# Kernel tuning notes

Measured on AMD Instinct MI355X. Metric: run time of the kernel, lower is better.

Reference implementation:

```python
import jax, jax.numpy as jnp
import numpy as np

B, T, L, W = 4, 4096, 64, 8          # batch, text len, media tokens, max_window_per_audio
DIM, DIM_A, H, DH = 2048, 1024, 8, 64
INNER = H * DH
LN_EPS = 1e-5


def setup_inputs() -> dict:
    key = jax.random.key(0)
    ks = jax.random.split(key, 8)
    x = jax.random.normal(ks[0], (B, T, DIM), jnp.float32)
    media = jax.random.normal(ks[1], (B, L, 1, DIM_A), jnp.float32)
    media_mask = jax.random.uniform(ks[2], (B, L, 1)) > 0.1
    # sparse media markers (~8 per row); ensure at least one per row
    media_locations = (jax.random.uniform(ks[3], (B, T)) < (8.0 / T)).astype(jnp.int32)
    media_locations = media_locations.at[:, 0].set(1)
    Wq = jax.random.normal(ks[4], (DIM, INNER), jnp.float32) / np.sqrt(DIM).astype(np.float32)
    Wkv = jax.random.normal(ks[5], (DIM_A, 2 * INNER), jnp.float32) / np.sqrt(DIM_A).astype(np.float32)
    Wout = jax.random.normal(ks[6], (INNER, DIM), jnp.float32) / np.sqrt(INNER).astype(np.float32)
    gamma = jnp.ones((DIM,), jnp.float32)
    beta = jnp.zeros((DIM,), jnp.float32)
    return dict(x=x, media=media, media_mask=media_mask, media_locations=media_locations,
                Wq=Wq, Wkv=Wkv, Wout=Wout, gamma=gamma, beta=beta)


def reference(x, media, media_mask, media_locations, Wq, Wkv, Wout, gamma, beta):
    scale = DH ** -0.5
    # LayerNorm (biased variance, like torch)
    mu = x.mean(-1, keepdims=True)
    var = x.var(-1, keepdims=True)
    xn = (x - mu) * jax.lax.rsqrt(var + LN_EPS) * gamma + beta
    # projections
    q = (xn @ Wq).reshape(B, T, H, DH).transpose(0, 2, 1, 3) * scale   # [B,h,T,dh]
    kv = media.reshape(B, L, DIM_A) @ Wkv
    k, v = jnp.split(kv, 2, axis=-1)
    k = k.reshape(B, L, H, DH).transpose(0, 2, 1, 3)                   # [B,h,L,dh]
    v = v.reshape(B, L, H, DH).transpose(0, 2, 1, 3)
    sim = jnp.einsum('bhid,bhjd->bhij', q, k)                          # [B,h,T,L]
    big = jnp.finfo(sim.dtype).max
    # media validity mask
    mm = media_mask.reshape(B, 1, 1, L)
    sim = jnp.where(mm, sim, -big)
    # few-shot window mask (only_attend_immediate_media=False):
    # token t attends windows [0, max(#media at <=t, 1) * W)
    cum = jnp.cumsum((media_locations != 0).astype(jnp.int32), axis=1)  # [B,T]
    end = jnp.maximum(cum, 1) * W                                       # [B,T]
    fsm = jnp.arange(L)[None, None, :] < end[:, :, None]                # [B,T,L]
    sim = jnp.where(fsm[:, None], sim, -big)
    sim = sim - jax.lax.stop_gradient(sim.max(-1, keepdims=True))
    attn = jax.nn.softmax(sim, axis=-1)
    out = jnp.einsum('bhij,bhjd->bhid', attn, v)                        # [B,h,T,dh]
    out = out.transpose(0, 2, 1, 3).reshape(B, T, INNER)
    return out @ Wout
```

## Files before the change

kernel.cpp:

```cpp
#include <hip/hip_runtime.h>
#include <float.h>

typedef __bf16 bf16;
typedef __bf16 bf16x8 __attribute__((ext_vector_type(8)));
typedef float f32x4 __attribute__((ext_vector_type(4)));

#define GAS __attribute__((address_space(1)))
#define LAS __attribute__((address_space(3)))

__device__ __forceinline__ void gload_lds16(const void* g, void* l) {
  __builtin_amdgcn_global_load_lds((const GAS unsigned int*)g, (LAS unsigned int*)l, 16, 0, 0);
}

__global__ __launch_bounds__(512, 4) void qattn(
    const bf16* __restrict__ xn, const bf16* __restrict__ wqT,
    const bf16* __restrict__ kvb, const int* __restrict__ mk,
    const int* __restrict__ endw, bf16* __restrict__ aob) {
  constexpr int K = 2048;
  __shared__ __align__(16) bf16 Abuf[2][128 * 64];
  __shared__ __align__(16) bf16 Bbuf[2][128 * 64];
  const int tid = threadIdx.x, lane = tid & 63;
  const int w = tid >> 6, wr = w >> 1, wc = w & 1;
  const int g = lane >> 4, fr = lane & 15;

  const int gx = gridDim.x;
  int lid = blockIdx.y * gx + blockIdx.x;
  lid = ((lid & 7) << 6) | (lid >> 3);
  const int bx = lid % gx, by = lid / gx;
  const size_t m0 = (size_t)by * 128;
  const int n0 = bx * 128;
  const int b = by >> 5;

  const int nt = K >> 6;
  const int srow = tid >> 3, sslot = tid & 7;

  f32x4 acc[2][4] = {};

  auto stage = [&](int t) {
    const int s = t & 1;
    const int kt = t << 6;
#pragma unroll
    for (int c = 0; c < 2; ++c) {
      const int r = c * 64 + srow;
      gload_lds16(xn + (m0 + r) * (size_t)K + kt + ((sslot ^ (r & 7)) << 3),
                  &Abuf[s][c * 4096 + tid * 8]);
    }
#pragma unroll
    for (int c = 0; c < 2; ++c) {
      const int r = c * 64 + srow;
      gload_lds16(wqT + (size_t)(n0 + r) * K + kt + ((sslot ^ (r & 7)) << 3),
                  &Bbuf[s][c * 4096 + tid * 8]);
    }
  };
  auto rdA = [&](int s, int mi, int ks) {
    const int r = wr * 32 + mi * 16 + fr;
    return *(const bf16x8*)&Abuf[s][r * 64 + ((((ks << 2) | g) ^ (r & 7)) << 3)];
  };
  auto rdB = [&](int s, int ni, int ks) {
    const int r = wc * 64 + ni * 16 + fr;
    return *(const bf16x8*)&Bbuf[s][r * 64 + ((((ks << 2) | g) ^ (r & 7)) << 3)];
  };
  auto compute = [&](int t) {
    const int s = t & 1;
    bf16x8 bv[4][2];
#pragma unroll
    for (int ni = 0; ni < 4; ++ni)
#pragma unroll
      for (int ks = 0; ks < 2; ++ks) bv[ni][ks] = rdB(s, ni, ks);
    __builtin_amdgcn_s_setprio(1);
#pragma unroll
    for (int mi = 0; mi < 2; ++mi)
#pragma unroll
      for (int ks = 0; ks < 2; ++ks) {
        const bf16x8 av = rdA(s, mi, ks);
#pragma unroll
        for (int ni = 0; ni < 4; ++ni)
          acc[mi][ni] = __builtin_amdgcn_mfma_f32_16x16x32_bf16(
              av, bv[ni][ks], acc[mi][ni], 0, 0, 0);
      }
    __builtin_amdgcn_s_setprio(0);
  };

  stage(0);
  for (int t = 0; t < nt; ++t) {
    __syncthreads();
    if (t + 1 < nt) stage(t + 1);
    compute(t);
  }

  __syncthreads();

  bf16* QP = &Abuf[0][0] + w * 2048;
  bf16* Klds = &Bbuf[0][0];
  bf16* Vlds = &Bbuf[1][0];

#pragma unroll
  for (int mi = 0; mi < 2; ++mi)
#pragma unroll
    for (int ni = 0; ni < 4; ++ni)
#pragma unroll
      for (int rg = 0; rg < 4; ++rg) {
        const int row = mi * 16 + g * 4 + rg, col = ni * 16 + fr;
        QP[row * 64 + (((col >> 3) ^ (row & 7)) << 3) + (col & 7)] =
            (bf16)acc[mi][ni][rg];
      }

#pragma unroll
  for (int j = 0; j < 2; ++j) {
    const int idx = j * 512 + tid;
    const int head = idx >> 9, l = (idx >> 3) & 63, sl = idx & 7;
    gload_lds16(kvb + (size_t)(b * 64 + l) * 1024 + (2 * bx + head) * 64 +
                    ((sl ^ (l & 7)) << 3),
                Klds + (j * 512 + w * 64) * 8);
  }
#pragma unroll
  for (int j = 0; j < 2; ++j) {
    const int idx = j * 512 + tid;
    const int head = idx >> 9, l = (idx >> 3) & 63, sg = idx & 7;
    bf16x8 vv = *(const bf16x8*)&kvb[(size_t)(b * 64 + l) * 1024 + 512 +
                                     (2 * bx + head) * 64 + sg * 8];
#pragma unroll
    for (int e = 0; e < 8; ++e) {
      const int dh = sg * 8 + e;
      Vlds[head * 4096 + dh * 64 + (((l >> 3) ^ (dh & 7)) << 3) + (l & 7)] =
          vv[e];
    }
  }
  asm volatile("s_waitcnt vmcnt(0)" ::: "memory");
  __syncthreads();

  f32x4 sacc[2][4] = {};
#pragma unroll
  for (int ks = 0; ks < 2; ++ks) {
    bf16x8 aq[2], bk[4];
#pragma unroll
    for (int mi = 0; mi < 2; ++mi) {
      const int r = mi * 16 + fr;
      aq[mi] = *(const bf16x8*)&QP[r * 64 + ((((ks << 2) | g) ^ (r & 7)) << 3)];
    }
#pragma unroll
    for (int ni = 0; ni < 4; ++ni) {
      const int l = ni * 16 + fr;
      bk[ni] = *(const bf16x8*)&Klds[wc * 4096 + l * 64 +
                                     ((((ks << 2) | g) ^ (l & 7)) << 3)];
    }
#pragma unroll
    for (int mi = 0; mi < 2; ++mi)
#pragma unroll
      for (int ni = 0; ni < 4; ++ni)
        sacc[mi][ni] = __builtin_amdgcn_mfma_f32_16x16x32_bf16(
            aq[mi], bk[ni], sacc[mi][ni], 0, 0, 0);
  }

#pragma unroll
  for (int mi = 0; mi < 2; ++mi) {
    const int4 ev4 = *(const int4*)&endw[m0 + wr * 32 + mi * 16 + g * 4];
    const int ev[4] = {ev4.x, ev4.y, ev4.z, ev4.w};
    float p[4][4];
#pragma unroll
    for (int ni = 0; ni < 4; ++ni) {
      const int l = ni * 16 + fr;
      const bool mv = (mk[b * 64 + l] != 0);
#pragma unroll
      for (int rg = 0; rg < 4; ++rg)
        p[ni][rg] = (mv && (l < ev[rg])) ? sacc[mi][ni][rg] : -FLT_MAX;
    }
#pragma unroll
    for (int rg = 0; rg < 4; ++rg) {
      float m = fmaxf(fmaxf(p[0][rg], p[1][rg]), fmaxf(p[2][rg], p[3][rg]));
      m = fmaxf(m, __shfl_xor(m, 1));
      m = fmaxf(m, __shfl_xor(m, 2));
      m = fmaxf(m, __shfl_xor(m, 4));
      m = fmaxf(m, __shfl_xor(m, 8));
      float sum = 0.f;
#pragma unroll
      for (int ni = 0; ni < 4; ++ni) {
        p[ni][rg] = __expf(p[ni][rg] - m);
        sum += p[ni][rg];
      }
      sum += __shfl_xor(sum, 1);
      sum += __shfl_xor(sum, 2);
      sum += __shfl_xor(sum, 4);
      sum += __shfl_xor(sum, 8);
      const float inv = 1.f / sum;
#pragma unroll
      for (int ni = 0; ni < 4; ++ni) p[ni][rg] *= inv;
    }
#pragma unroll
    for (int ni = 0; ni < 4; ++ni) {
      const int l = ni * 16 + fr;
#pragma unroll
      for (int rg = 0; rg < 4; ++rg) {
        const int row = mi * 16 + g * 4 + rg;
        QP[row * 64 + (((l >> 3) ^ (row & 7)) << 3) + (l & 7)] =
            (bf16)p[ni][rg];
      }
    }
  }

  f32x4 oacc[2][4] = {};
#pragma unroll
  for (int ks = 0; ks < 2; ++ks) {
    bf16x8 pa[2], bv[4];
#pragma unroll
    for (int mi = 0; mi < 2; ++mi) {
      const int r = mi * 16 + fr;
      pa[mi] = *(const bf16x8*)&QP[r * 64 + ((((ks << 2) | g) ^ (r & 7)) << 3)];
    }
#pragma unroll
    for (int nd = 0; nd < 4; ++nd) {
      const int dh = nd * 16 + fr;
      bv[nd] = *(const bf16x8*)&Vlds[wc * 4096 + dh * 64 +
                                     ((((ks << 2) | g) ^ (dh & 7)) << 3)];
    }
#pragma unroll
    for (int mi = 0; mi < 2; ++mi)
#pragma unroll
      for (int nd = 0; nd < 4; ++nd)
        oacc[mi][nd] = __builtin_amdgcn_mfma_f32_16x16x32_bf16(
            pa[mi], bv[nd], oacc[mi][nd], 0, 0, 0);
  }
#pragma unroll
  for (int mi = 0; mi < 2; ++mi)
#pragma unroll
    for (int nd = 0; nd < 4; ++nd)
#pragma unroll
      for (int rg = 0; rg < 4; ++rg) {
        const size_t t = m0 + wr * 32 + mi * 16 + g * 4 + rg;
        aob[t * 512 + (2 * bx + wc) * 64 + nd * 16 + fr] =
            (bf16)oacc[mi][nd][rg];
      }
}

template <int OUT_BF16>
__global__ __launch_bounds__(256, 2) void gemm_bt(
    const bf16* __restrict__ A, const bf16* __restrict__ Bt,
    void* __restrict__ Cv, int M, int N, int K) {
  __shared__ bf16 As[128 * 32];
  __shared__ bf16 Bs[128 * 32];
  const int tid = threadIdx.x;
  const int lane = tid & 63, w = tid >> 6;
  const int wr = w >> 1, wc = w & 1;

  const int gx = gridDim.x;
  const int nwg = gx * gridDim.y;
  int lid = blockIdx.y * gx + blockIdx.x;
  {
    const int qq = nwg >> 3, rr = nwg & 7;
    const int xcd = lid & 7, pos = lid >> 3;
    lid = (xcd < rr ? xcd * (qq + 1) : rr * (qq + 1) + (xcd - rr) * qq) + pos;
  }
  const int bx = lid % gx, by = lid / gx;
  const size_t m0 = (size_t)by * 128, n0 = (size_t)bx * 128;

  const int srow = lane >> 2, sslot = lane & 3;
  const int g = lane >> 4, fr = lane & 15;

  f32x4 acc[4][4] = {};

  for (int kt = 0; kt < K; kt += 32) {
    __syncthreads();
#pragma unroll
    for (int j = 0; j < 2; ++j) {
      const int c = 2 * w + j;
      const int r = c * 16 + srow;
      const int ks = (sslot ^ (r & 3)) << 3;
      gload_lds16(A + (m0 + r) * K + kt + ks, &As[c * 512]);
      gload_lds16(Bt + (n0 + r) * K + kt + ks, &Bs[c * 512]);
    }
    __syncthreads();
    bf16x8 av[4], bv[4];
#pragma unroll
    for (int mi = 0; mi < 4; ++mi) {
      const int r = wr * 64 + mi * 16 + fr;
      av[mi] = *(const bf16x8*)&As[r * 32 + ((g ^ (r & 3)) << 3)];
    }
#pragma unroll
    for (int ni = 0; ni < 4; ++ni) {
      const int r = wc * 64 + ni * 16 + fr;
      bv[ni] = *(const bf16x8*)&Bs[r * 32 + ((g ^ (r & 3)) << 3)];
    }
#pragma unroll
    for (int mi = 0; mi < 4; ++mi)
#pragma unroll
      for (int ni = 0; ni < 4; ++ni)
        acc[mi][ni] = __builtin_amdgcn_mfma_f32_16x16x32_bf16(
            av[mi], bv[ni], acc[mi][ni], 0, 0, 0);
  }

#pragma unroll
  for (int mi = 0; mi < 4; ++mi)
#pragma unroll
    for (int ni = 0; ni < 4; ++ni)
#pragma unroll
      for (int rg = 0; rg < 4; ++rg) {
        const size_t row = m0 + wr * 64 + mi * 16 + g * 4 + rg;
        const size_t col = n0 + wc * 64 + ni * 16 + fr;
        if (OUT_BF16)
          ((bf16*)Cv)[row * (size_t)N + col] = (bf16)acc[mi][ni][rg];
        else
          ((float*)Cv)[row * (size_t)N + col] = acc[mi][ni][rg];
      }
}

__device__ __forceinline__ void transp64(const float* __restrict__ src,
                                         bf16* __restrict__ dst, int R, int C,
                                         float scale, int tile, float* lds) {
  const int tilesC = C >> 6;
  const int tr = tile / tilesC, tc = tile % tilesC;
  const int r0 = tr << 6, c0 = tc << 6;
  const int tid = threadIdx.x;
  const int lr = tid >> 6, lc = tid & 63;
#pragma unroll
  for (int j = 0; j < 16; ++j) {
    const int r = j * 4 + lr;
    lds[r * 65 + lc] = src[(size_t)(r0 + r) * C + c0 + lc];
  }
  __syncthreads();
#pragma unroll
  for (int j = 0; j < 16; ++j) {
    const int rr = j * 4 + lr;
    dst[(size_t)(c0 + rr) * R + r0 + lc] = (bf16)(lds[lc * 65 + rr] * scale);
  }
}

__global__ __launch_bounds__(256) void prep_all(
    const float* __restrict__ x, const float* __restrict__ gamma,
    const float* __restrict__ beta, bf16* __restrict__ xn,
    const float* __restrict__ Wq, bf16* __restrict__ wqT,
    const float* __restrict__ Wkv, bf16* __restrict__ wkvT,
    const float* __restrict__ Wout, bf16* __restrict__ woT,
    const float* __restrict__ media, bf16* __restrict__ medb,
    const int* __restrict__ mloc, int* __restrict__ endw,
    const unsigned char* __restrict__ mraw, int* __restrict__ mk) {
  __shared__ float shf[64 * 65];
  const int blk = blockIdx.x, tid = threadIdx.x;

  if (blk < 16384) {
    const size_t base = (size_t)blk * 2048 + tid * 8;
    f32x4 v0 = *(const f32x4*)(x + base);
    f32x4 v1 = *(const f32x4*)(x + base + 4);
    float s = 0.f, q2 = 0.f;
#pragma unroll
    for (int j = 0; j < 4; ++j) {
      s += v0[j] + v1[j];
      q2 += v0[j] * v0[j] + v1[j] * v1[j];
    }
    for (int off = 32; off > 0; off >>= 1) {
      s += __shfl_down(s, off);
      q2 += __shfl_down(q2, off);
    }
    const int lane = tid & 63, wv = tid >> 6;
    if (lane == 0) { shf[wv] = s; shf[4 + wv] = q2; }
    __syncthreads();
    s = shf[0] + shf[1] + shf[2] + shf[3];
    q2 = shf[4] + shf[5] + shf[6] + shf[7];
    const float mu = s * (1.f / 2048.f);
    const float var = q2 * (1.f / 2048.f) - mu * mu;
    const float rs = rsqrtf(var + 1e-5f);
    f32x4 g0 = *(const f32x4*)(gamma + tid * 8);
    f32x4 g1 = *(const f32x4*)(gamma + tid * 8 + 4);
    f32x4 b0 = *(const f32x4*)(beta + tid * 8);
    f32x4 b1 = *(const f32x4*)(beta + tid * 8 + 4);
    bf16x8 o;
#pragma unroll
    for (int j = 0; j < 4; ++j) {
      o[j] = (bf16)((v0[j] - mu) * rs * g0[j] + b0[j]);
      o[4 + j] = (bf16)((v1[j] - mu) * rs * g1[j] + b1[j]);
    }
    *(bf16x8*)(xn + base) = o;
  } else if (blk < 16640) {
    transp64(Wq, wqT, 2048, 512, 0.125f, blk - 16384, shf);
  } else if (blk < 16896) {
    transp64(Wkv, wkvT, 1024, 1024, 1.f, blk - 16640, shf);
  } else if (blk < 17152) {
    transp64(Wout, woT, 512, 2048, 1.f, blk - 16896, shf);
  } else if (blk < 18176) {
    const int i = (blk - 17152) * 256 + tid;
    medb[i] = (bf16)media[i];
  } else if (blk < 18180) {
    int* part = (int*)shf;
    const int b = blk - 18176;
    int loc[16];
    int s = 0;
    const int base = b * 4096 + tid * 16;
#pragma unroll
    for (int j = 0; j < 16; ++j) {
      loc[j] = (mloc[base + j] != 0) ? 1 : 0;
      s += loc[j];
    }
    part[tid] = s;
    __syncthreads();
    for (int off = 1; off < 256; off <<= 1) {
      int v = (tid >= off) ? part[tid - off] : 0;
      __syncthreads();
      part[tid] += v;
      __syncthreads();
    }
    int c = (tid > 0) ? part[tid - 1] : 0;
#pragma unroll
    for (int j = 0; j < 16; ++j) {
      c += loc[j];
      int e = (c > 1 ? c : 1) << 3;
      endw[base + j] = e > 64 ? 64 : e;
    }
  } else {
    int* isbool = (int*)shf;
    if (tid == 0) *isbool = 0;
    __syncthreads();
    const unsigned char v = mraw[tid];
    if ((tid & 3) != 0 && v != 0) atomicOr(isbool, 1);
    __syncthreads();
    mk[tid] = (*isbool) ? (int)mraw[tid] : ((const int*)mraw)[tid];
  }
}

extern "C" void kernel_launch(void* const* d_in, const int* in_sizes, int n_in,
                              void* d_out, int out_size, void* d_ws,
                              size_t ws_size, hipStream_t stream) {
  const float* x = (const float*)d_in[0];
  const float* media = (const float*)d_in[1];
  const unsigned char* mraw = (const unsigned char*)d_in[2];
  const int* mloc = (const int*)d_in[3];
  const float* Wq = (const float*)d_in[4];
  const float* Wkv = (const float*)d_in[5];
  const float* Wout = (const float*)d_in[6];
  const float* gamma = (const float*)d_in[7];
  const float* beta = (const float*)d_in[8];
  float* out = (float*)d_out;

  bf16* xn = (bf16*)d_out;

  char* ws = (char*)d_ws;
  size_t off = 0;
  auto carve = [&](size_t bytes) {
    void* p = ws + off;
    off += (bytes + 255) & ~(size_t)255;
    return p;
  };
  bf16* aob = (bf16*)carve((size_t)16384 * 512 * 2);
  bf16* kvb = (bf16*)carve((size_t)256 * 1024 * 2);
  bf16* wqT = (bf16*)carve((size_t)512 * 2048 * 2);
  bf16* wkvT = (bf16*)carve((size_t)1024 * 1024 * 2);
  bf16* woT = (bf16*)carve((size_t)2048 * 512 * 2);
  bf16* medb = (bf16*)carve((size_t)256 * 1024 * 2);
  int* endw = (int*)carve((size_t)4 * 4096 * 4);
  int* mk = (int*)carve(256 * 4);
  (void)ws_size;
  (void)in_sizes;
  (void)n_in;
  (void)out_size;

  prep_all<<<18181, 256, 0, stream>>>(x, gamma, beta, xn, Wq, wqT, Wkv, wkvT,
                                      Wout, woT, media, medb, mloc, endw, mraw,
                                      mk);

  gemm_bt<1><<<dim3(8, 2), 256, 0, stream>>>(medb, wkvT, kvb, 256, 1024, 1024);

  qattn<<<dim3(4, 128), 512, 0, stream>>>(xn, wqT, kvb, mk, endw, aob);

  gemm_bt<0><<<dim3(16, 128), 256, 0, stream>>>(aob, woT, out, 16384, 2048,
                                                512);
}
```

Before: 158.0 us.

## Replace output projection GEMM with double-buffered LDS-DMA MFMA kernel

Adds a new output-projection GEMM kernel that uses 512 threads, 64-wide K tiles, double-buffered shared memory filled with direct global-to-LDS loads, XOR-swizzled layout and 16x16x32 bf16 MFMA, and launches it instead of the generic gemm_bt. The aim is to overlap global loads with MFMA compute and cut LDS bank conflicts and sync overhead in the largest GEMM (16384x2048x512). The cost is higher shared memory per block (64 KB), which may limit occupancy, and an fp32 store pattern that writes one scalar per lane.

After: 159.7 us. Within noise of the previous version (+1.1%).

```diff
diff --git a/kernel.cpp b/kernel.cpp
--- a/kernel.cpp
+++ b/kernel.cpp
@@ -229,6 +229,91 @@
         const size_t t = m0 + wr * 32 + mi * 16 + g * 4 + rg;
         aob[t * 512 + (2 * bx + wc) * 64 + nd * 16 + fr] =
             (bf16)oacc[mi][nd][rg];
+      }
+}
+
+__global__ __launch_bounds__(512, 4) void gemm_out(
+    const bf16* __restrict__ A, const bf16* __restrict__ Bt,
+    float* __restrict__ C, int M, int N, int K) {
+  __shared__ __align__(16) bf16 Abuf[2][128 * 64];
+  __shared__ __align__(16) bf16 Bbuf[2][128 * 64];
+  const int tid = threadIdx.x, lane = tid & 63;
+  const int w = tid >> 6, wr = w >> 1, wc = w & 1;
+  const int g = lane >> 4, fr = lane & 15;
+
+  const int gx = gridDim.x;
+  const int nwg = gx * gridDim.y;
+  int lid = blockIdx.y * gx + blockIdx.x;
+  {
+    const int qq = nwg >> 3;
+    lid = (lid & 7) * qq + (lid >> 3);
+  }
+  const int bx = lid % gx, by = lid / gx;
+  const size_t m0 = (size_t)by * 128, n0 = (size_t)bx * 128;
+
+  const int nt = K >> 6;
+  const int srow = tid >> 3, sslot = tid & 7;
+
+  f32x4 acc[2][4] = {};
+
+  auto stage = [&](int t) {
+    const int s = t & 1;
+    const int kt = t << 6;
+#pragma unroll
+    for (int c = 0; c < 2; ++c) {
+      const int r = c * 64 + srow;
+      gload_lds16(A + (m0 + r) * (size_t)K + kt + ((sslot ^ (r & 7)) << 3),
+                  &Abuf[s][c * 4096 + tid * 8]);
+    }
+#pragma unroll
+    for (int c = 0; c < 2; ++c) {
+      const int r = c * 64 + srow;
+      gload_lds16(Bt + (n0 + r) * (size_t)K + kt + ((sslot ^ (r & 7)) << 3),
+                  &Bbuf[s][c * 4096 + tid * 8]);
+    }
+  };
+  auto rdA = [&](int s, int mi, int ks) {
+    const int r = wr * 32 + mi * 16 + fr;
+    return *(const bf16x8*)&Abuf[s][r * 64 + ((((ks << 2) | g) ^ (r & 7)) << 3)];
+  };
+  auto rdB = [&](int s, int ni, int ks) {
+    const int r = wc * 64 + ni * 16 + fr;
+    return *(const bf16x8*)&Bbuf[s][r * 64 + ((((ks << 2) | g) ^ (r & 7)) << 3)];
+  };
+
+  stage(0);
+  for (int t = 0; t < nt; ++t) {
+    __syncthreads();
+    if (t + 1 < nt) stage(t + 1);
+    const int s = t & 1;
+    bf16x8 bv[4][2];
+#pragma unroll
+    for (int ni = 0; ni < 4; ++ni)
+#pragma unroll
+      for (int ks = 0; ks < 2; ++ks) bv[ni][ks] = rdB(s, ni, ks);
+    __builtin_amdgcn_s_setprio(1);
+#pragma unroll
+    for (int mi = 0; mi < 2; ++mi)
+#pragma unroll
+      for (int ks = 0; ks < 2; ++ks) {
+        const bf16x8 av = rdA(s, mi, ks);
+#pragma unroll
+        for (int ni = 0; ni < 4; ++ni)
+          acc[mi][ni] = __builtin_amdgcn_mfma_f32_16x16x32_bf16(
+              av, bv[ni][ks], acc[mi][ni], 0, 0, 0);
+      }
+    __builtin_amdgcn_s_setprio(0);
+  }
+
+#pragma unroll
+  for (int mi = 0; mi < 2; ++mi)
+#pragma unroll
+    for (int ni = 0; ni < 4; ++ni)
+#pragma unroll
+      for (int rg = 0; rg < 4; ++rg) {
+        const size_t row = m0 + wr * 32 + mi * 16 + g * 4 + rg;
+        const size_t col = n0 + wc * 64 + ni * 16 + fr;
+        C[row * (size_t)N + col] = acc[mi][ni][rg];
       }
 }
 
@@ -459,6 +544,5 @@
 
   qattn<<<dim3(4, 128), 512, 0, stream>>>(xn, wqT, kvb, mk, endw, aob);
 
-  gemm_bt<0><<<dim3(16, 128), 256, 0, stream>>>(aob, woT, out, 16384, 2048,
-                                                512);
-}
+  gemm_out<<<dim3(16, 128), 512, 0, stream>>>(aob, woT, out, 16384, 2048, 512);
+}
```

## Shrink fused Q-attention blocks to 64 rows and reuse shared memory

Applied to the files above, without the earlier changes.

The fused Q-projection plus attention kernel now uses 256-thread blocks, each covering 64 token rows instead of 128, with a K-step of 32 instead of 64. The grid doubles to 1024 blocks. Shared memory drops to about 40KB: the A/B stage buffers are carved from one smaller array, and a single epilogue buffer is reused first for K and then for transposed V, with extra barriers in between. The aim is more resident blocks per CU and better latency hiding, at the cost of twice as many K-loop iterations, less operand reuse per block, and serialized K then V loading.

Result: slower. 178.8 us (+13.2%).

```diff
diff --git a/kernel.cpp b/kernel.cpp
--- a/kernel.cpp
+++ b/kernel.cpp
@@ -12,72 +12,71 @@
   __builtin_amdgcn_global_load_lds((const GAS unsigned int*)g, (LAS unsigned int*)l, 16, 0, 0);
 }
 
-__global__ __launch_bounds__(512, 4) void qattn(
+__global__ __launch_bounds__(256, 4) void qattn(
     const bf16* __restrict__ xn, const bf16* __restrict__ wqT,
     const bf16* __restrict__ kvb, const int* __restrict__ mk,
     const int* __restrict__ endw, bf16* __restrict__ aob) {
   constexpr int K = 2048;
-  __shared__ __align__(16) bf16 Abuf[2][128 * 64];
-  __shared__ __align__(16) bf16 Bbuf[2][128 * 64];
+  __shared__ __align__(16) bf16 SM[12288];
+  __shared__ __align__(16) bf16 Ep[8192];
   const int tid = threadIdx.x, lane = tid & 63;
   const int w = tid >> 6, wr = w >> 1, wc = w & 1;
   const int g = lane >> 4, fr = lane & 15;
 
   const int gx = gridDim.x;
   int lid = blockIdx.y * gx + blockIdx.x;
-  lid = ((lid & 7) << 6) | (lid >> 3);
+  lid = ((lid & 7) << 7) | (lid >> 3);
   const int bx = lid % gx, by = lid / gx;
-  const size_t m0 = (size_t)by * 128;
+  const size_t m0 = (size_t)by * 64;
   const int n0 = bx * 128;
-  const int b = by >> 5;
-
-  const int nt = K >> 6;
-  const int srow = tid >> 3, sslot = tid & 7;
+  const int b = by >> 6;
+
+  const int nt = K >> 5;
+  const int srow = tid >> 2, sslot = tid & 3;
+
+  auto Abuf = [&](int s) { return SM + s * 2048; };
+  auto Bbuf = [&](int s) { return SM + 4096 + s * 4096; };
 
   f32x4 acc[2][4] = {};
 
   auto stage = [&](int t) {
     const int s = t & 1;
-    const int kt = t << 6;
-#pragma unroll
-    for (int c = 0; c < 2; ++c) {
-      const int r = c * 64 + srow;
-      gload_lds16(xn + (m0 + r) * (size_t)K + kt + ((sslot ^ (r & 7)) << 3),
-                  &Abuf[s][c * 4096 + tid * 8]);
-    }
-#pragma unroll
-    for (int c = 0; c < 2; ++c) {
-      const int r = c * 64 + srow;
-      gload_lds16(wqT + (size_t)(n0 + r) * K + kt + ((sslot ^ (r & 7)) << 3),
-                  &Bbuf[s][c * 4096 + tid * 8]);
+    const int kt = t << 5;
+    {
+      const int r = srow;
+      gload_lds16(xn + (m0 + r) * (size_t)K + kt + ((sslot ^ (r & 3)) << 3),
+                  Abuf(s) + tid * 8);
+    }
+#pragma unroll
+    for (int j = 0; j < 2; ++j) {
+      const int idx = j * 256 + tid;
+      const int r = idx >> 2, sl = idx & 3;
+      gload_lds16(wqT + (size_t)(n0 + r) * K + kt + ((sl ^ (r & 3)) << 3),
+                  Bbuf(s) + idx * 8);
     }
   };
-  auto rdA = [&](int s, int mi, int ks) {
+  auto rdA = [&](int s, int mi) {
     const int r = wr * 32 + mi * 16 + fr;
-    return *(const bf16x8*)&Abuf[s][r * 64 + ((((ks << 2) | g) ^ (r & 7)) << 3)];
+    return *(const bf16x8*)(Abuf(s) + r * 32 + ((g ^ (r & 3)) << 3));
   };
-  auto rdB = [&](int s, int ni, int ks) {
+  auto rdB = [&](int s, int ni) {
     const int r = wc * 64 + ni * 16 + fr;
-    return *(const bf16x8*)&Bbuf[s][r * 64 + ((((ks << 2) | g) ^ (r & 7)) << 3)];
+    return *(const bf16x8*)(Bbuf(s) + r * 32 + ((g ^ (r & 3)) << 3));
   };
   auto compute = [&](int t) {
     const int s = t & 1;
-    bf16x8 bv[4][2];
-#pragma unroll
-    for (int ni = 0; ni < 4; ++ni)
-#pragma unroll
-      for (int ks = 0; ks < 2; ++ks) bv[ni][ks] = rdB(s, ni, ks);
+    bf16x8 bv[4];
+#pragma unroll
+    for (int ni = 0; ni < 4; ++ni) bv[ni] = rdB(s, ni);
     __builtin_amdgcn_s_setprio(1);
 #pragma unroll
-    for (int mi = 0; mi < 2; ++mi)
-#pragma unroll
-      for (int ks = 0; ks < 2; ++ks) {
-        const bf16x8 av = rdA(s, mi, ks);
-#pragma unroll
-        for (int ni = 0; ni < 4; ++ni)
-          acc[mi][ni] = __builtin_amdgcn_mfma_f32_16x16x32_bf16(
-              av, bv[ni][ks], acc[mi][ni], 0, 0, 0);
-      }
+    for (int mi = 0; mi < 2; ++mi) {
+      const bf16x8 av = rdA(s, mi);
+#pragma unroll
+      for (int ni = 0; ni < 4; ++ni)
+        acc[mi][ni] = __builtin_amdgcn_mfma_f32_16x16x32_bf16(
+            av, bv[ni], acc[mi][ni], 0, 0, 0);
+    }
     __builtin_amdgcn_s_setprio(0);
   };
 
@@ -90,9 +89,7 @@
 
   __syncthreads();
 
-  bf16* QP = &Abuf[0][0] + w * 2048;
-  bf16* Klds = &Bbuf[0][0];
-  bf16* Vlds = &Bbuf[1][0];
+  bf16* QP = SM + w * 2048;
 
 #pragma unroll
   for (int mi = 0; mi < 2; ++mi)
@@ -106,50 +103,53 @@
       }
 
 #pragma unroll
-  for (int j = 0; j < 2; ++j) {
-    const int idx = j * 512 + tid;
+  for (int j = 0; j < 4; ++j) {
+    const int idx = j * 256 + tid;
     const int head = idx >> 9, l = (idx >> 3) & 63, sl = idx & 7;
     gload_lds16(kvb + (size_t)(b * 64 + l) * 1024 + (2 * bx + head) * 64 +
                     ((sl ^ (l & 7)) << 3),
-                Klds + (j * 512 + w * 64) * 8);
-  }
-#pragma unroll
-  for (int j = 0; j < 2; ++j) {
-    const int idx = j * 512 + tid;
+                Ep + idx * 8);
+  }
+  asm volatile("s_waitcnt vmcnt(0)" ::: "memory");
+  __syncthreads();
+
+  f32x4 sacc[2][4] = {};
+#pragma unroll
+  for (int ks = 0; ks < 2; ++ks) {
+    bf16x8 aq[2], bk[4];
+#pragma unroll
+    for (int mi = 0; mi < 2; ++mi) {
+      const int r = mi * 16 + fr;
+      aq[mi] = *(const bf16x8*)&QP[r * 64 + ((((ks << 2) | g) ^ (r & 7)) << 3)];
+    }
+#pragma unroll
+    for (int ni = 0; ni < 4; ++ni) {
+      const int l = ni * 16 + fr;
+      bk[ni] = *(const bf16x8*)&Ep[wc * 4096 + l * 64 +
+                                   ((((ks << 2) | g) ^ (l & 7)) << 3)];
+    }
+#pragma unroll
+    for (int mi = 0; mi < 2; ++mi)
+#pragma unroll
+      for (int ni = 0; ni < 4; ++ni)
+        sacc[mi][ni] = __builtin_amdgcn_mfma_f32_16x16x32_bf16(
+            aq[mi], bk[ni], sacc[mi][ni], 0, 0, 0);
+  }
+
+  __syncthreads();
+
+#pragma unroll
+  for (int j = 0; j < 4; ++j) {
+    const int idx = j * 256 + tid;
     const int head = idx >> 9, l = (idx >> 3) & 63, sg = idx & 7;
     bf16x8 vv = *(const bf16x8*)&kvb[(size_t)(b * 64 + l) * 1024 + 512 +
                                      (2 * bx + head) * 64 + sg * 8];
 #pragma unroll
     for (int e = 0; e < 8; ++e) {
       const int dh = sg * 8 + e;
-      Vlds[head * 4096 + dh * 64 + (((l >> 3) ^ (dh & 7)) << 3) + (l & 7)] =
+      Ep[head * 4096 + dh * 64 + (((l >> 3) ^ (dh & 7)) << 3) + (l & 7)] =
           vv[e];
     }
-  }
-  asm volatile("s_waitcnt vmcnt(0)" ::: "memory");
-  __syncthreads();
-
-  f32x4 sacc[2][4] = {};
-#pragma unroll
-  for (int ks = 0; ks < 2; ++ks) {
-    bf16x8 aq[2], bk[4];
-#pragma unroll
-    for (int mi = 0; mi < 2; ++mi) {
-      const int r = mi * 16 + fr;
-      aq[mi] = *(const bf16x8*)&QP[r * 64 + ((((ks << 2) | g) ^ (r & 7)) << 3)];
-    }
-#pragma unroll
-    for (int ni = 0; ni < 4; ++ni) {
-      const int l = ni * 16 + fr;
-      bk[ni] = *(const bf16x8*)&Klds[wc * 4096 + l * 64 +
-                                     ((((ks << 2) | g) ^ (l & 7)) << 3)];
-    }
-#pragma unroll
-    for (int mi = 0; mi < 2; ++mi)
-#pragma unroll
-      for (int ni = 0; ni < 4; ++ni)
-        sacc[mi][ni] = __builtin_amdgcn_mfma_f32_16x16x32_bf16(
-            aq[mi], bk[ni], sacc[mi][ni], 0, 0, 0);
   }
 
 #pragma unroll
@@ -198,6 +198,8 @@
     }
   }
 
+  __syncthreads();
+
   f32x4 oacc[2][4] = {};
 #pragma unroll
   for (int ks = 0; ks < 2; ++ks) {
@@ -210,8 +212,8 @@
 #pragma unroll
     for (int nd = 0; nd < 4; ++nd) {
       const int dh = nd * 16 + fr;
-      bv[nd] = *(const bf16x8*)&Vlds[wc * 4096 + dh * 64 +
-                                     ((((ks << 2) | g) ^ (dh & 7)) << 3)];
+      bv[nd] = *(const bf16x8*)&Ep[wc * 4096 + dh * 64 +
+                                   ((((ks << 2) | g) ^ (dh & 7)) << 3)];
     }
 #pragma unroll
     for (int mi = 0; mi < 2; ++mi)
@@ -457,7 +459,7 @@
 
   gemm_bt<1><<<dim3(8, 2), 256, 0, stream>>>(medb, wkvT, kvb, 256, 1024, 1024);
 
-  qattn<<<dim3(4, 128), 512, 0, stream>>>(xn, wqT, kvb, mk, endw, aob);
+  qattn<<<dim3(4, 256), 256, 0, stream>>>(xn, wqT, kvb, mk, endw, aob);
 
   gemm_bt<0><<<dim3(16, 128), 256, 0, stream>>>(aob, woT, out, 16384, 2048,
                                                 512);
```
